# Kernel tuning notes

Measured on AMD Instinct MI355X. Metric: run time of the kernel, lower is better.

The kernel has to match this reference:

```python
import jax, jax.numpy as jnp
import numpy as np

WS = 11
SIGMA = 1.5
CH = 3
C1 = (0.01 * 255.0) ** 2  # 6.5025
C2 = (0.03 * 255.0) ** 2  # 58.5225


def _gauss_window():
    # 1D Gaussian -> outer product -> depthwise kernel [C, 1, ws, ws] (OIHW)
    coords = jnp.arange(WS, dtype=jnp.float32) - WS // 2
    g = jnp.exp(-coords ** 2 / (2.0 * SIGMA ** 2))
    g = g / g.sum()
    w2d = g[:, None] * g[None, :]
    return jnp.tile(w2d[None, None], (CH, 1, 1, 1))


def _dwconv(x, win):
    pad = WS // 2
    return jax.lax.conv_general_dilated(
        x, win, window_strides=(1, 1), padding=[(pad, pad), (pad, pad)],
        feature_group_count=CH,
        dimension_numbers=('NCHW', 'OIHW', 'NCHW'))


def setup_inputs() -> dict:
    key = jax.random.key(0)
    k1, k2 = jax.random.split(key)
    shape = (32, 3, 512, 512)
    img_gen = jax.random.uniform(k1, shape, jnp.float32, -1.0, 1.0)
    img_ref = jax.random.uniform(k2, shape, jnp.float32, -1.0, 1.0)
    return {"img_gen": img_gen, "img_ref": img_ref}


def reference(img_gen, img_ref):
    gen = (img_gen + 1.0) * 0.5
    ref = (img_ref + 1.0) * 0.5
    win = _gauss_window()

    mu1 = _dwconv(gen, win)
    mu2 = _dwconv(ref, win)
    mu1_sq = mu1 * mu1
    mu2_sq = mu2 * mu2
    mu1_mu2 = mu1 * mu2
    sigma1_sq = _dwconv(gen * gen, win) - mu1_sq
    sigma2_sq = _dwconv(ref * ref, win) - mu2_sq
    sigma12 = _dwconv(gen * ref, win) - mu1_mu2

    ssim_map = ((2.0 * mu1_mu2 + C1) * (2.0 * sigma12 + C2)) / (
        (mu1_sq + mu2_sq + C1) * (sigma1_sq + sigma2_sq + C2))
    return 1.0 - ssim_map.mean()
```

## Files before the change

kernel.cpp:

```cpp
#include <hip/hip_runtime.h>

typedef float v2f __attribute__((ext_vector_type(2)));

#define TX 64
#define TY 20
#define WIN 30
#define RING 30
#define HSTR 65
#define IMW 512
#define IMH 512
#define NPLANES 96
#define NBX (IMW / TX)
#define NCHUNK ((IMH + TY - 1) / TY)
#define NBLOCKS (NBX * NPLANES)

#define GW0 0.00102838f
#define GW1 0.00759877f
#define GW2 0.03600077f
#define GW3 0.10936069f
#define GW4 0.21300553f
#define GW5 0.26601172f

__device__ __forceinline__ void pkfma(v2f& acc, v2f a, v2f b) {
  asm("v_pk_fma_f32 %0, %1, %2, %0" : "+v"(acc) : "v"(a), "v"(b));
}
__device__ __forceinline__ v2f pkmul(v2f a, v2f b) {
  v2f d;
  asm("v_pk_mul_f32 %0, %1, %2" : "=v"(d) : "v"(a), "v"(b));
  return d;
}

__device__ __forceinline__ void hblur(
    const float* __restrict__ gp, const float* __restrict__ rp,
    float* __restrict__ sq, int x0, bool interior_x,
    int nrows, int gy0, int slot0, int tid) {
  if (tid >= nrows * 8) return;
  const float GW[11] = {GW0, GW1, GW2, GW3, GW4, GW5,
                        GW4, GW3, GW2, GW1, GW0};
  const int r = tid >> 3;
  const int xs = (tid & 7) * 8;
  const int gy = gy0 + r;
  int slot = slot0 + r;
  if (slot >= RING) slot -= RING;
  const int xbase = x0 + xs - 8;
  const float* grow = gp + (size_t)gy * IMW;
  const float* rrow = rp + (size_t)gy * IMW;

  v2f P[24];
  const bool rowok = (gy >= 0) & (gy < IMH);
  if (interior_x & rowok) {
#pragma unroll
    for (int k = 0; k < 6; ++k) {
      const int c = xbase + 4 * k;
      const float4 g4 = *(const float4*)(grow + c);
      const float4 r4 = *(const float4*)(rrow + c);
      P[4 * k + 0] = (v2f){fmaf(0.5f, g4.x, 0.5f), fmaf(0.5f, r4.x, 0.5f)};
      P[4 * k + 1] = (v2f){fmaf(0.5f, g4.y, 0.5f), fmaf(0.5f, r4.y, 0.5f)};
      P[4 * k + 2] = (v2f){fmaf(0.5f, g4.z, 0.5f), fmaf(0.5f, r4.z, 0.5f)};
      P[4 * k + 3] = (v2f){fmaf(0.5f, g4.w, 0.5f), fmaf(0.5f, r4.w, 0.5f)};
    }
  } else {
#pragma unroll
    for (int k = 0; k < 6; ++k) {
      const int c = xbase + 4 * k;
      const bool ok = rowok && (c >= 0) && (c < IMW);
      float4 g4 = make_float4(-1.f, -1.f, -1.f, -1.f);
      float4 r4 = g4;
      if (ok) {
        g4 = *(const float4*)(grow + c);
        r4 = *(const float4*)(rrow + c);
      }
      P[4 * k + 0] = (v2f){fmaf(0.5f, g4.x, 0.5f), fmaf(0.5f, r4.x, 0.5f)};
      P[4 * k + 1] = (v2f){fmaf(0.5f, g4.y, 0.5f), fmaf(0.5f, r4.y, 0.5f)};
      P[4 * k + 2] = (v2f){fmaf(0.5f, g4.z, 0.5f), fmaf(0.5f, r4.z, 0.5f)};
      P[4 * k + 3] = (v2f){fmaf(0.5f, g4.w, 0.5f), fmaf(0.5f, r4.w, 0.5f)};
    }
  }

  v2f accP[8], accQ[8];
  float accS[8];
#pragma unroll
  for (int o = 0; o < 8; ++o) {
    accP[o] = (v2f){0.f, 0.f};
    accQ[o] = (v2f){0.f, 0.f};
    accS[o] = 0.f;
  }

#pragma unroll
  for (int p = 0; p < 18; ++p) {
    const v2f pv = P[p + 3];
    const v2f qv = pkmul(pv, pv);
    const float sv = pv.x * pv.y;
    const int olo = (p - 10 < 0) ? 0 : p - 10;
    const int ohi = (p < 7) ? p : 7;
#pragma unroll
    for (int o = olo; o <= ohi; ++o) {
      const float wt = GW[p - o];
      const v2f wv = (v2f){wt, wt};
      pkfma(accP[o], wv, pv);
      pkfma(accQ[o], wv, qv);
      accS[o] = fmaf(wt, sv, accS[o]);
    }
  }

  float* dst = sq + slot * (5 * HSTR) + xs;
#pragma unroll
  for (int o = 0; o < 8; ++o) dst[0 * HSTR + o] = accP[o].x;
#pragma unroll
  for (int o = 0; o < 8; ++o) dst[1 * HSTR + o] = accP[o].y;
#pragma unroll
  for (int o = 0; o < 8; ++o) dst[2 * HSTR + o] = accQ[o].x;
#pragma unroll
  for (int o = 0; o < 8; ++o) dst[3 * HSTR + o] = accQ[o].y;
#pragma unroll
  for (int o = 0; o < 8; ++o) dst[4 * HSTR + o] = accS[o];
}

__global__ __launch_bounds__(256, 4) void ssim_main(
    const float* __restrict__ gen, const float* __restrict__ ref,
    double* __restrict__ partial) {
  __shared__ float s_q[RING][5][HSTR];
  __shared__ double swsum[4];

  const float GW[11] = {GW0, GW1, GW2, GW3, GW4, GW5,
                        GW4, GW3, GW2, GW1, GW0};

  const int tid = threadIdx.x;
  const int bid = blockIdx.x;
  const int bx = bid & (NBX - 1);
  const int plane = bid >> 3;
  const int x0 = bx * TX;
  const float* gp = gen + (size_t)plane * (IMW * IMH);
  const float* rp = ref + (size_t)plane * (IMW * IMH);
  const bool interior_x = (bx >= 1) & (bx <= NBX - 2);

  const int col = tid & 63;
  const int r0 = __builtin_amdgcn_readfirstlane((tid >> 6) * 5);

  double acc = 0.0;

  hblur(gp, rp, &s_q[0][0][0], x0, interior_x, WIN, -5, 0, tid);

  int base = 0;
  for (int c = 0; c < NCHUNK; ++c) {
    if (c > 0) {
      int s0 = base + 10;
      if (s0 >= RING) s0 -= RING;
      hblur(gp, rp, &s_q[0][0][0], x0, interior_x, TY, TY * c + 5, s0, tid);
    }
    __syncthreads();

    int b2 = base + r0;
    if (b2 >= RING) b2 -= RING;
    v2f hp[15], hq[15];
    float hs[15];
#pragma unroll
    for (int i = 0; i < 15; ++i) {
      int slot = b2 + i;
      if (slot >= RING) slot -= RING;
      const float* rowp = &s_q[slot][0][col];
      hp[i] = (v2f){rowp[0 * HSTR], rowp[1 * HSTR]};
      hq[i] = (v2f){rowp[2 * HSTR], rowp[3 * HSTR]};
      hs[i] = rowp[4 * HSTR];
    }

    const float C1 = 6.5025f, C2 = 58.5225f;
    float lsum = 0.f;
#pragma unroll
    for (int o = 0; o < 5; ++o) {
      v2f mu = (v2f){0.f, 0.f};
      v2f ee = (v2f){0.f, 0.f};
      float e12 = 0.f;
#pragma unroll
      for (int t = 0; t < 11; ++t) {
        const float wt = GW[t];
        const v2f wv = (v2f){wt, wt};
        pkfma(mu, wv, hp[o + t]);
        pkfma(ee, wv, hq[o + t]);
        e12 = fmaf(wt, hs[o + t], e12);
      }
      const float mu1 = mu.x, mu2 = mu.y, e1 = ee.x, e2 = ee.y;
      const float m12 = mu1 * mu2;
      const float m1s = mu1 * mu1;
      const float m2s = mu2 * mu2;
      const float num = (2.f * m12 + C1) * (2.f * (e12 - m12) + C2);
      const float den = (m1s + m2s + C1) * ((e1 - m1s) + (e2 - m2s) + C2);
      const int y = TY * c + r0 + o;
      lsum += (y < IMH) ? __fdividef(num, den) : 0.f;
    }
    acc += (double)lsum;

    __syncthreads();
    base += TY;
    if (base >= RING) base -= RING;
  }

#pragma unroll
  for (int off = 32; off > 0; off >>= 1) acc += __shfl_down(acc, off, 64);
  if ((tid & 63) == 0) swsum[tid >> 6] = acc;
  __syncthreads();
  if (tid == 0) partial[bid] = swsum[0] + swsum[1] + swsum[2] + swsum[3];
}

__global__ void ssim_reduce(const double* __restrict__ partial,
                            float* __restrict__ out) {
  const int tid = threadIdx.x;
  double s = partial[tid] + partial[tid + 256] + partial[tid + 512];
#pragma unroll
  for (int off = 32; off > 0; off >>= 1) s += __shfl_down(s, off, 64);
  __shared__ double sd[4];
  if ((tid & 63) == 0) sd[tid >> 6] = s;
  __syncthreads();
  if (tid == 0) {
    const double npix = (double)NPLANES * (double)IMW * (double)IMH;
    out[0] = (float)(1.0 - (sd[0] + sd[1] + sd[2] + sd[3]) / npix);
  }
}

extern "C" void kernel_launch(void* const* d_in, const int* in_sizes, int n_in,
                              void* d_out, int out_size, void* d_ws, size_t ws_size,
                              hipStream_t stream) {
  (void)in_sizes; (void)n_in; (void)out_size; (void)ws_size;
  const float* gen = (const float*)d_in[0];
  const float* ref = (const float*)d_in[1];
  double* partial = (double*)d_ws;
  ssim_main<<<NBLOCKS, 256, 0, stream>>>(gen, ref, partial);
  ssim_reduce<<<1, 256, 0, stream>>>(partial, (float*)d_out);
}
```

Measured before the change: 314.2 us.

## Split image rows across blocks and prefetch next chunk's loads before compute

Each block now handles a 40-row strip (two 20-row chunks) instead of a whole 512-row column strip, multiplying the grid by about thirteen so many more blocks are available to fill the GPU. The horizontal pass is split into a load stage and a compute stage, so global loads for the second chunk are issued before the first chunk's vertical pass runs and their latency is hidden. In exchange, each block reloads a 10-row halo, which adds redundant global reads and horizontal-blur work (about 50 rows loaded per 40 output rows), and the reduce kernel now loops over more partials.

New measurement: 278.9 us. 1.13x faster.

```diff
diff --git a/kernel.cpp b/kernel.cpp
--- a/kernel.cpp
+++ b/kernel.cpp
@@ -4,15 +4,16 @@
 
 #define TX 64
 #define TY 20
+#define MY 2
+#define BYR (TY * MY)
 #define WIN 30
-#define RING 30
 #define HSTR 65
 #define IMW 512
 #define IMH 512
 #define NPLANES 96
 #define NBX (IMW / TX)
-#define NCHUNK ((IMH + TY - 1) / TY)
-#define NBLOCKS (NBX * NPLANES)
+#define NBY ((IMH + BYR - 1) / BYR)
+#define NBLOCKS (NBX * NBY * NPLANES)
 
 #define GW0 0.00102838f
 #define GW1 0.00759877f
@@ -30,36 +31,29 @@
   return d;
 }
 
-__device__ __forceinline__ void hblur(
+struct Raw {
+  float4 g[6];
+  float4 r[6];
+};
+
+__device__ __forceinline__ void hload(
     const float* __restrict__ gp, const float* __restrict__ rp,
-    float* __restrict__ sq, int x0, bool interior_x,
-    int nrows, int gy0, int slot0, int tid) {
+    int x0, bool fast, int nrows, int gy0, int tid, Raw& L) {
   if (tid >= nrows * 8) return;
-  const float GW[11] = {GW0, GW1, GW2, GW3, GW4, GW5,
-                        GW4, GW3, GW2, GW1, GW0};
   const int r = tid >> 3;
   const int xs = (tid & 7) * 8;
   const int gy = gy0 + r;
-  int slot = slot0 + r;
-  if (slot >= RING) slot -= RING;
   const int xbase = x0 + xs - 8;
   const float* grow = gp + (size_t)gy * IMW;
   const float* rrow = rp + (size_t)gy * IMW;
-
-  v2f P[24];
-  const bool rowok = (gy >= 0) & (gy < IMH);
-  if (interior_x & rowok) {
+  if (fast) {
 #pragma unroll
     for (int k = 0; k < 6; ++k) {
-      const int c = xbase + 4 * k;
-      const float4 g4 = *(const float4*)(grow + c);
-      const float4 r4 = *(const float4*)(rrow + c);
-      P[4 * k + 0] = (v2f){fmaf(0.5f, g4.x, 0.5f), fmaf(0.5f, r4.x, 0.5f)};
-      P[4 * k + 1] = (v2f){fmaf(0.5f, g4.y, 0.5f), fmaf(0.5f, r4.y, 0.5f)};
-      P[4 * k + 2] = (v2f){fmaf(0.5f, g4.z, 0.5f), fmaf(0.5f, r4.z, 0.5f)};
-      P[4 * k + 3] = (v2f){fmaf(0.5f, g4.w, 0.5f), fmaf(0.5f, r4.w, 0.5f)};
+      L.g[k] = *(const float4*)(grow + xbase + 4 * k);
+      L.r[k] = *(const float4*)(rrow + xbase + 4 * k);
     }
   } else {
+    const bool rowok = (gy >= 0) & (gy < IMH);
 #pragma unroll
     for (int k = 0; k < 6; ++k) {
       const int c = xbase + 4 * k;
@@ -70,11 +64,31 @@
         g4 = *(const float4*)(grow + c);
         r4 = *(const float4*)(rrow + c);
       }
-      P[4 * k + 0] = (v2f){fmaf(0.5f, g4.x, 0.5f), fmaf(0.5f, r4.x, 0.5f)};
-      P[4 * k + 1] = (v2f){fmaf(0.5f, g4.y, 0.5f), fmaf(0.5f, r4.y, 0.5f)};
-      P[4 * k + 2] = (v2f){fmaf(0.5f, g4.z, 0.5f), fmaf(0.5f, r4.z, 0.5f)};
-      P[4 * k + 3] = (v2f){fmaf(0.5f, g4.w, 0.5f), fmaf(0.5f, r4.w, 0.5f)};
-    }
+      L.g[k] = g4;
+      L.r[k] = r4;
+    }
+  }
+}
+
+__device__ __forceinline__ void hcompute(
+    const Raw& L, float* __restrict__ sq, int nrows, int slot0, int tid) {
+  if (tid >= nrows * 8) return;
+  const float GW[11] = {GW0, GW1, GW2, GW3, GW4, GW5,
+                        GW4, GW3, GW2, GW1, GW0};
+  const int r = tid >> 3;
+  const int xs = (tid & 7) * 8;
+  int slot = slot0 + r;
+  if (slot >= WIN) slot -= WIN;
+
+  v2f P[24];
+#pragma unroll
+  for (int k = 0; k < 6; ++k) {
+    const float4 g4 = L.g[k];
+    const float4 r4 = L.r[k];
+    P[4 * k + 0] = (v2f){fmaf(0.5f, g4.x, 0.5f), fmaf(0.5f, r4.x, 0.5f)};
+    P[4 * k + 1] = (v2f){fmaf(0.5f, g4.y, 0.5f), fmaf(0.5f, r4.y, 0.5f)};
+    P[4 * k + 2] = (v2f){fmaf(0.5f, g4.z, 0.5f), fmaf(0.5f, r4.z, 0.5f)};
+    P[4 * k + 3] = (v2f){fmaf(0.5f, g4.w, 0.5f), fmaf(0.5f, r4.w, 0.5f)};
   }
 
   v2f accP[8], accQ[8];
@@ -116,84 +130,89 @@
   for (int o = 0; o < 8; ++o) dst[4 * HSTR + o] = accS[o];
 }
 
+__device__ __forceinline__ float phase2(
+    const float* __restrict__ sq, int winbase, int ybase, int col, int r0) {
+  const float GW[11] = {GW0, GW1, GW2, GW3, GW4, GW5,
+                        GW4, GW3, GW2, GW1, GW0};
+  v2f hp[15], hq[15];
+  float hs[15];
+#pragma unroll
+  for (int i = 0; i < 15; ++i) {
+    int slot = winbase + r0 + i;
+    if (slot >= WIN) slot -= WIN;
+    const float* rowp = sq + slot * (5 * HSTR) + col;
+    hp[i] = (v2f){rowp[0 * HSTR], rowp[1 * HSTR]};
+    hq[i] = (v2f){rowp[2 * HSTR], rowp[3 * HSTR]};
+    hs[i] = rowp[4 * HSTR];
+  }
+
+  const float C1 = 6.5025f, C2 = 58.5225f;
+  float lsum = 0.f;
+#pragma unroll
+  for (int o = 0; o < 5; ++o) {
+    v2f mu = (v2f){0.f, 0.f};
+    v2f ee = (v2f){0.f, 0.f};
+    float e12 = 0.f;
+#pragma unroll
+    for (int t = 0; t < 11; ++t) {
+      const float wt = GW[t];
+      const v2f wv = (v2f){wt, wt};
+      pkfma(mu, wv, hp[o + t]);
+      pkfma(ee, wv, hq[o + t]);
+      e12 = fmaf(wt, hs[o + t], e12);
+    }
+    const float mu1 = mu.x, mu2 = mu.y, e1 = ee.x, e2 = ee.y;
+    const float m12 = mu1 * mu2;
+    const float m1s = mu1 * mu1;
+    const float m2s = mu2 * mu2;
+    const float num = (2.f * m12 + C1) * (2.f * (e12 - m12) + C2);
+    const float den = (m1s + m2s + C1) * ((e1 - m1s) + (e2 - m2s) + C2);
+    const int y = ybase + r0 + o;
+    lsum += (y < IMH) ? __fdividef(num, den) : 0.f;
+  }
+  return lsum;
+}
+
 __global__ __launch_bounds__(256, 4) void ssim_main(
     const float* __restrict__ gen, const float* __restrict__ ref,
     double* __restrict__ partial) {
-  __shared__ float s_q[RING][5][HSTR];
+  __shared__ float s_q[WIN][5][HSTR];
   __shared__ double swsum[4];
-
-  const float GW[11] = {GW0, GW1, GW2, GW3, GW4, GW5,
-                        GW4, GW3, GW2, GW1, GW0};
+  float* const sq = &s_q[0][0][0];
 
   const int tid = threadIdx.x;
   const int bid = blockIdx.x;
   const int bx = bid & (NBX - 1);
-  const int plane = bid >> 3;
+  const int rem = bid >> 3;
+  const int by = rem % NBY;
+  const int plane = rem / NBY;
   const int x0 = bx * TX;
+  const int Y0 = by * BYR;
   const float* gp = gen + (size_t)plane * (IMW * IMH);
   const float* rp = ref + (size_t)plane * (IMW * IMH);
-  const bool interior_x = (bx >= 1) & (bx <= NBX - 2);
+  const bool ix = (bx >= 1) & (bx <= NBX - 2);
 
   const int col = tid & 63;
   const int r0 = __builtin_amdgcn_readfirstlane((tid >> 6) * 5);
 
-  double acc = 0.0;
-
-  hblur(gp, rp, &s_q[0][0][0], x0, interior_x, WIN, -5, 0, tid);
-
-  int base = 0;
-  for (int c = 0; c < NCHUNK; ++c) {
-    if (c > 0) {
-      int s0 = base + 10;
-      if (s0 >= RING) s0 -= RING;
-      hblur(gp, rp, &s_q[0][0][0], x0, interior_x, TY, TY * c + 5, s0, tid);
-    }
-    __syncthreads();
-
-    int b2 = base + r0;
-    if (b2 >= RING) b2 -= RING;
-    v2f hp[15], hq[15];
-    float hs[15];
-#pragma unroll
-    for (int i = 0; i < 15; ++i) {
-      int slot = b2 + i;
-      if (slot >= RING) slot -= RING;
-      const float* rowp = &s_q[slot][0][col];
-      hp[i] = (v2f){rowp[0 * HSTR], rowp[1 * HSTR]};
-      hq[i] = (v2f){rowp[2 * HSTR], rowp[3 * HSTR]};
-      hs[i] = rowp[4 * HSTR];
-    }
-
-    const float C1 = 6.5025f, C2 = 58.5225f;
-    float lsum = 0.f;
-#pragma unroll
-    for (int o = 0; o < 5; ++o) {
-      v2f mu = (v2f){0.f, 0.f};
-      v2f ee = (v2f){0.f, 0.f};
-      float e12 = 0.f;
-#pragma unroll
-      for (int t = 0; t < 11; ++t) {
-        const float wt = GW[t];
-        const v2f wv = (v2f){wt, wt};
-        pkfma(mu, wv, hp[o + t]);
-        pkfma(ee, wv, hq[o + t]);
-        e12 = fmaf(wt, hs[o + t], e12);
-      }
-      const float mu1 = mu.x, mu2 = mu.y, e1 = ee.x, e2 = ee.y;
-      const float m12 = mu1 * mu2;
-      const float m1s = mu1 * mu1;
-      const float m2s = mu2 * mu2;
-      const float num = (2.f * m12 + C1) * (2.f * (e12 - m12) + C2);
-      const float den = (m1s + m2s + C1) * ((e1 - m1s) + (e2 - m2s) + C2);
-      const int y = TY * c + r0 + o;
-      lsum += (y < IMH) ? __fdividef(num, den) : 0.f;
-    }
-    acc += (double)lsum;
-
-    __syncthreads();
-    base += TY;
-    if (base >= RING) base -= RING;
-  }
+  Raw L0;
+  hload(gp, rp, x0, ix & (Y0 - 5 >= 0) & (Y0 + 25 <= IMH), WIN, Y0 - 5, tid, L0);
+  hcompute(L0, sq, WIN, 0, tid);
+
+  Raw L1;
+  hload(gp, rp, x0, ix & (Y0 + 45 <= IMH), TY, Y0 + 25, tid, L1);
+
+  __syncthreads();
+
+  double acc = (double)phase2(sq, 0, Y0, col, r0);
+
+  __syncthreads();
+
+  hcompute(L1, sq, TY, 0, tid);
+
+  __syncthreads();
+
+  acc += (double)phase2(sq, 20, Y0 + TY, col, r0);
 
 #pragma unroll
   for (int off = 32; off > 0; off >>= 1) acc += __shfl_down(acc, off, 64);
@@ -205,7 +224,8 @@
 __global__ void ssim_reduce(const double* __restrict__ partial,
                             float* __restrict__ out) {
   const int tid = threadIdx.x;
-  double s = partial[tid] + partial[tid + 256] + partial[tid + 512];
+  double s = 0.0;
+  for (int i = tid; i < NBLOCKS; i += 256) s += partial[i];
 #pragma unroll
   for (int off = 32; off > 0; off >>= 1) s += __shfl_down(s, off, 64);
   __shared__ double sd[4];
```
